# Kernel optimization log

Measured on AMD Instinct MI355X. Metric: run time of the kernel, lower is better.

The kernel has to match this reference:

```python
import jax, jax.numpy as jnp
import numpy as np

B, S, H, NH = 1, 2048, 4096, 32
HD = H // NH
INV_NORM = 1.0 / float(np.sqrt(HD))
BETA = 1.0
NEG_MIN = float(np.finfo(np.float32).min)


def setup_inputs() -> dict:
    key = jax.random.key(0)
    ks = jax.random.split(key, 8)
    hidden_states = jax.random.normal(ks[0], (B, S, H), dtype=jnp.float32)
    residual = jax.random.normal(ks[1], (B, S, H), dtype=jnp.float32)
    # ALiBi: per-head slope * position, shape [B*NH, 1, S] as HF BLOOM builds it
    slopes = jnp.asarray(2.0 ** (-8.0 * (np.arange(1, NH + 1) / NH)), dtype=jnp.float32)
    pos = jnp.arange(S, dtype=jnp.float32)
    alibi = (slopes[:, None, None] * pos[None, None, :])  # [NH,1,S]
    alibi = jnp.tile(alibi, (B, 1, 1))  # [B*NH,1,S]
    # causal mask: True where attention is NOT allowed
    attention_mask = jnp.triu(jnp.ones((S, S), dtype=bool), k=1)[None, None]  # [1,1,S,S]
    w_qkv = jax.random.normal(ks[2], (3 * H, H), dtype=jnp.float32) * 0.02
    b_qkv = jax.random.normal(ks[3], (3 * H,), dtype=jnp.float32) * 0.02
    w_dense = jax.random.normal(ks[4], (H, H), dtype=jnp.float32) * 0.02
    b_dense = jax.random.normal(ks[5], (H,), dtype=jnp.float32) * 0.02
    return {
        'hidden_states': hidden_states, 'residual': residual, 'alibi': alibi,
        'attention_mask': attention_mask, 'w_qkv': w_qkv, 'b_qkv': b_qkv,
        'w_dense': w_dense, 'b_dense': b_dense,
    }


def reference(hidden_states, residual, alibi, attention_mask, w_qkv, b_qkv, w_dense, b_dense):
    # fused QKV projection, interleaved per-head split as in BLOOM
    fused = hidden_states @ w_qkv.T + b_qkv  # [B,S,3H]
    fused = fused.reshape(B, S, NH, 3, HD)
    q, k, v = fused[..., 0, :], fused[..., 1, :], fused[..., 2, :]  # [B,S,NH,HD]
    # baddbmm: beta*alibi + alpha * Q K^T
    scores = jnp.einsum('bqhd,bkhd->bhqk', q, k) * INV_NORM  # [B,NH,S,S]
    scores = scores + BETA * alibi.reshape(B, NH, 1, S)
    scores = jnp.where(attention_mask, NEG_MIN, scores)
    probs = jax.nn.softmax(scores, axis=-1)  # fp32 softmax (inputs already fp32)
    ctx = jnp.einsum('bhqk,bkhd->bqhd', probs, v).reshape(B, S, H)
    out = ctx @ w_dense.T + b_dense
    return out + residual  # dropout_add with p=0 in eval
```

## Files before the change

### kernel.cpp

```cpp
#include <hip/hip_runtime.h>
#include <cstdint>
#include <cstddef>

#define S_LEN 2048
#define H_DIM 4096
#define NHEAD 32
#define HD    128
#define N_QKV 12288
#define INV_NORM 0.08838834764831845f

typedef __bf16 bf16_t;
typedef bf16_t bf16x8 __attribute__((ext_vector_type(8)));
typedef bf16_t bf16x4 __attribute__((ext_vector_type(4)));
typedef float  f32x4  __attribute__((ext_vector_type(4)));

static_assert(sizeof(bf16x8) == 16, "bf16x8 must be 16B");

__device__ __forceinline__ f32x4 mfma16(bf16x8 a, bf16x8 b, f32x4 c) {
  return __builtin_amdgcn_mfma_f32_16x16x32_bf16(a, b, c, 0, 0, 0);
}

typedef __attribute__((address_space(1))) void gas_void;
typedef __attribute__((address_space(3))) void las_void;
__device__ __forceinline__ void async16(const void* g, void* l) {
  __builtin_amdgcn_global_load_lds((const gas_void*)g,
                                   (las_void*)(uint32_t)(uintptr_t)l,
                                   16, 0, 0);
}

#define SWZ(x)    ((x) ^ ((((x) >> 7) & 7) << 4))
#define SWZ256(x) ((x) ^ ((((x) >> 8) & 7) << 4))
#define VMCNT(n) asm volatile("s_waitcnt vmcnt(" #n ")" ::: "memory")
#define LGKM0()  asm volatile("s_waitcnt lgkmcnt(0)" ::: "memory")
#define SCHED0() __builtin_amdgcn_sched_barrier(0)
#define BARRIER() __builtin_amdgcn_s_barrier()

typedef float f32v4 __attribute__((ext_vector_type(4)));
#define NX4 ((S_LEN * H_DIM) / 4)
#define NQ4 ((N_QKV * H_DIM) / 4)
#define ND4 ((H_DIM * H_DIM) / 4)
__global__ void cvt_all(const float* __restrict__ x, const float* __restrict__ wq,
                        const float* __restrict__ wd,
                        bf16_t* __restrict__ xb, bf16_t* __restrict__ wqb,
                        bf16_t* __restrict__ wdb) {
  int i = blockIdx.x * 256 + threadIdx.x;
  const float* src; bf16_t* dst; int j;
  if (i < NX4) { src = x; dst = xb; j = i; }
  else if (i < NX4 + NQ4) { src = wq; dst = wqb; j = i - NX4; }
  else if (i < NX4 + NQ4 + ND4) { src = wd; dst = wdb; j = i - NX4 - NQ4; }
  else return;
  f32v4 v = ((const f32v4*)src)[j];
  bf16x4 r;
  r[0] = (bf16_t)v[0]; r[1] = (bf16_t)v[1]; r[2] = (bf16_t)v[2]; r[3] = (bf16_t)v[3];
  ((bf16x4*)dst)[j] = r;
}

template <int MODE, int BN>
__global__ __launch_bounds__(512, 2)
void gemm_pipe(const bf16_t* __restrict__ Ag,
               const bf16_t* __restrict__ Bg,
               const float* __restrict__ bias,
               const float* __restrict__ residual,
               bf16_t* __restrict__ q_out,
               bf16_t* __restrict__ k_out,
               bf16_t* __restrict__ v_out,
               float* __restrict__ f_out,
               int ncol)
{
  constexpr int NFRAG = BN / 32;
  constexpr int NBU   = BN / 64;
  constexpr int BBUF  = BN * 128;
  __shared__ __align__(16) char sm[65536 + 2 * BBUF];
  char* smA = sm;
  char* smB = sm + 65536;
  const int Kdim = H_DIM;
  const int NT = Kdim >> 6;

  const int tid = threadIdx.x, lane = tid & 63, w = tid >> 6;
  const int wm = w >> 1, wn = w & 1;
  const int lo = lane & 15, g = lane >> 4;

  const int nwg = gridDim.x * gridDim.y;
  const int bid = blockIdx.y * gridDim.x + blockIdx.x;
  const int cpx = nwg >> 3;
  const int sbid = (bid & 7) * cpx + (bid >> 3);
  const int brow = (sbid / ncol) << 8;
  const int bcol = (sbid % ncol) * BN;

  auto stageA = [&](int t, int u) {
    const int lin = u * 8192 + w * 1024 + lane * 16;
    const int lg = SWZ(lin);
    const bf16_t* src = Ag + (size_t)(brow + (lg >> 7)) * Kdim + (t << 6) + ((lg & 127) >> 1);
    async16(src, smA + ((t & 1) * 32768 + u * 8192 + w * 1024));
  };
  auto stageB = [&](int t, int u) {
    const int lin = u * 8192 + w * 1024 + lane * 16;
    const int lg = SWZ(lin);
    const bf16_t* src = Bg + (size_t)(bcol + (lg >> 7)) * Kdim + (t << 6) + ((lg & 127) >> 1);
    async16(src, smB + ((t & 1) * BBUF + u * 8192 + w * 1024));
  };
  auto rdA = [&](int t, int mi, int ks) -> bf16x8 {
    const int lin = (wm * 64 + mi * 16 + lo) * 128 + ks * 64 + g * 16;
    return *(const bf16x8*)(smA + (t & 1) * 32768 + SWZ(lin));
  };
  auto rdB = [&](int t, int ni, int ks) -> bf16x8 {
    const int lin = (wn * (BN / 2) + ni * 16 + lo) * 128 + ks * 64 + g * 16;
    return *(const bf16x8*)(smB + (t & 1) * BBUF + SWZ(lin));
  };

  f32x4 acc[4][NFRAG] = {};
  bf16x8 bfrag[NFRAG][2];

#pragma unroll
  for (int u = 0; u < NBU; ++u) stageB(0, u);
  stageA(0, 0); stageA(0, 1); stageA(0, 2); stageA(0, 3);
#pragma unroll
  for (int u = 0; u < NBU; ++u) stageB(1, u);
  if constexpr (NBU == 3) { VMCNT(3); } else { VMCNT(2); }
  SCHED0();
  BARRIER();

  for (int t = 0; t < NT; ++t) {
    bf16x8 afrag[2][2];
#pragma unroll
    for (int ni = 0; ni < NFRAG; ++ni)
#pragma unroll
      for (int ks = 0; ks < 2; ++ks)
        bfrag[ni][ks] = rdB(t, ni, ks);
#pragma unroll
    for (int j = 0; j < 2; ++j)
#pragma unroll
      for (int ks = 0; ks < 2; ++ks)
        afrag[j][ks] = rdA(t, j, ks);
    if (t + 1 < NT) { stageA(t + 1, 0); stageA(t + 1, 1); stageA(t + 1, 2); stageA(t + 1, 3); }
    SCHED0();
    BARRIER();
    __builtin_amdgcn_s_setprio(1);
#pragma unroll
    for (int j = 0; j < 2; ++j)
#pragma unroll
      for (int ni = 0; ni < NFRAG; ++ni)
#pragma unroll
        for (int ks = 0; ks < 2; ++ks)
          acc[j][ni] = mfma16(afrag[j][ks], bfrag[ni][ks], acc[j][ni]);
    __builtin_amdgcn_s_setprio(0);
    SCHED0();
    BARRIER();
#pragma unroll
    for (int j = 0; j < 2; ++j)
#pragma unroll
      for (int ks = 0; ks < 2; ++ks)
        afrag[j][ks] = rdA(t, 2 + j, ks);
    if (t + 2 < NT) {
#pragma unroll
      for (int u = 0; u < NBU; ++u) stageB(t + 2, u);
    }
    SCHED0();
    BARRIER();
    if (t < NT - 2) {
      if constexpr (NBU == 3) { VMCNT(3); } else { VMCNT(2); }
    } else if (t == NT - 2) {
      VMCNT(0);
    }
    __builtin_amdgcn_s_setprio(1);
#pragma unroll
    for (int j = 0; j < 2; ++j)
#pragma unroll
      for (int ni = 0; ni < NFRAG; ++ni)
#pragma unroll
        for (int ks = 0; ks < 2; ++ks)
          acc[2 + j][ni] = mfma16(afrag[j][ks], bfrag[ni][ks], acc[2 + j][ni]);
    __builtin_amdgcn_s_setprio(0);
    SCHED0();
    BARRIER();
  }

  if (MODE == 0) {
#pragma unroll
    for (int ni = 0; ni < NFRAG; ++ni) {
      const int cg = bcol + wn * (BN / 2) + ni * 16 + lo;
      const int chunk = cg >> 7;
      const int slot = chunk % 3, head = chunk / 3;
      bf16_t* dst = (slot == 0) ? q_out : (slot == 1) ? k_out : v_out;
      dst += (size_t)head * S_LEN * HD;
      const float scale = (slot == 0) ? INV_NORM : 1.0f;
      const float bb = bias[cg];
      const int d = cg & 127;
#pragma unroll
      for (int mi = 0; mi < 4; ++mi) {
#pragma unroll
        for (int jj = 0; jj < 4; ++jj) {
          const int r = brow + wm * 64 + mi * 16 + g * 4 + jj;
          dst[(size_t)r * HD + d] = (bf16_t)((acc[mi][ni][jj] + bb) * scale);
        }
      }
    }
  } else {
#pragma unroll
    for (int ni = 0; ni < NFRAG; ++ni) {
      const int cg = bcol + wn * (BN / 2) + ni * 16 + lo;
      const float bb = bias[cg];
#pragma unroll
      for (int mi = 0; mi < 4; ++mi) {
#pragma unroll
        for (int jj = 0; jj < 4; ++jj) {
          const int r = brow + wm * 64 + mi * 16 + g * 4 + jj;
          f_out[(size_t)r * H_DIM + cg] = acc[mi][ni][jj] + bb + residual[(size_t)r * H_DIM + cg];
        }
      }
    }
  }
}

__global__ __launch_bounds__(256, 2)
void attn_kernel(const bf16_t* __restrict__ Qg,
                 const bf16_t* __restrict__ Kg,
                 const bf16_t* __restrict__ Vg,
                 const float* __restrict__ alibi,
                 bf16_t* __restrict__ ctx)
{
  const int bid = blockIdx.x;
  const int h  = (bid & 7) * 4 + ((bid >> 3) & 3);
  const int qb = 31 - (bid >> 5);
  const int tid = threadIdx.x, lane = tid & 63, w = tid >> 6;
  const int lo = lane & 15, g = lane >> 4;

  __shared__ __align__(16) bf16_t Ks[2][64 * 128];
  __shared__ bf16_t Vt[2][128][72];
  __shared__ bf16_t Pl[4][16][72];

  const bf16_t* Qh = Qg + ((size_t)h * S_LEN + qb * 64 + w * 16) * HD;
  const bf16_t* Kh = Kg + (size_t)h * S_LEN * HD;
  const bf16_t* Vh = Vg + (size_t)h * S_LEN * HD;
  const float slope = alibi[(size_t)h * S_LEN + 1];

  bf16x8 qf[4];
#pragma unroll
  for (int ds = 0; ds < 4; ds++)
    qf[ds] = *(const bf16x8*)(Qh + lo * HD + ds * 32 + g * 8);

  f32x4 oacc[8] = {};
  float m_r[4], l_r[4];
#pragma unroll
  for (int jj = 0; jj < 4; jj++) { m_r[jj] = -INFINITY; l_r[jj] = 0.f; }

  const int ntiles = qb + 1;
  const int q_base = qb * 64 + w * 16;

  bf16x8 vvA[4], vvB[4];
#pragma unroll
  for (int u = 0; u < 4; ++u)
    vvA[u] = *(const bf16x8*)(Vh + (size_t)lane * HD + (u * 4 + w) * 8);
#pragma unroll
  for (int u = 0; u < 4; ++u) {
    const int lin = u * 4096 + tid * 16;
    const int lg = SWZ256(lin);
    async16(Kh + (size_t)(lg >> 8) * HD + ((lg & 255) >> 1),
            (char*)&Ks[0][0] + u * 4096 + w * 1024);
  }

  for (int kt = 0; kt < ntiles; ++kt) {
    const int k0 = kt * 64;
    const int cur = kt & 1;
    const bf16x8* vvC = cur ? vvB : vvA;
    bf16x8* vvN = cur ? vvA : vvB;

#pragma unroll
    for (int u = 0; u < 4; ++u) {
      const int d0 = (u * 4 + w) * 8;
#pragma unroll
      for (int e = 0; e < 8; ++e) Vt[cur][d0 + e][lane] = vvC[u][e];
    }
    if (kt + 1 < ntiles) {
      const bf16_t* Vn = Vh + (size_t)(k0 + 64) * HD;
#pragma unroll
      for (int u = 0; u < 4; ++u)
        vvN[u] = *(const bf16x8*)(Vn + (size_t)lane * HD + (u * 4 + w) * 8);
    }
    SCHED0();
    if (kt + 1 < ntiles) { VMCNT(4); } else { VMCNT(0); }
    LGKM0();
    SCHED0();
    BARRIER();
    SCHED0();
    if (kt + 1 < ntiles) {
      const bf16_t* Kn = Kh + (size_t)(k0 + 64) * HD;
#pragma unroll
      for (int u = 0; u < 4; ++u) {
        const int lin = u * 4096 + tid * 16;
        const int lg = SWZ256(lin);
        async16(Kn + (size_t)(lg >> 8) * HD + ((lg & 255) >> 1),
                (char*)&Ks[cur ^ 1][0] + u * 4096 + w * 1024);
      }
    }

    f32x4 sacc[4] = {};
#pragma unroll
    for (int kc = 0; kc < 4; ++kc) {
      bf16x8 kf[4];
#pragma unroll
      for (int ds = 0; ds < 4; ++ds) {
        const int lin = (kc * 16 + lo) * 256 + ds * 64 + g * 16;
        kf[ds] = *(const bf16x8*)((const char*)&Ks[cur][0] + SWZ256(lin));
      }
      __builtin_amdgcn_s_setprio(1);
#pragma unroll
      for (int ds = 0; ds < 4; ++ds)
        sacc[kc] = mfma16(qf[ds], kf[ds], sacc[kc]);
      __builtin_amdgcn_s_setprio(0);
    }

    float sv[4][4];
#pragma unroll
    for (int kc = 0; kc < 4; kc++) {
      const float alk = slope * (float)(k0 + kc * 16 + lo);
#pragma unroll
      for (int jj = 0; jj < 4; jj++)
        sv[kc][jj] = sacc[kc][jj] + alk;
    }
    if (kt == ntiles - 1) {
#pragma unroll
      for (int kc = 0; kc < 4; kc++) {
        const int k_gl = k0 + kc * 16 + lo;
#pragma unroll
        for (int jj = 0; jj < 4; jj++) {
          const int q_gl = q_base + g * 4 + jj;
          if (k_gl > q_gl) sv[kc][jj] = -INFINITY;
        }
      }
    }

#pragma unroll
    for (int jj = 0; jj < 4; jj++) {
      float mx = fmaxf(fmaxf(sv[0][jj], sv[1][jj]), fmaxf(sv[2][jj], sv[3][jj]));
      mx = fmaxf(mx, __shfl_xor(mx, 1, 64));
      mx = fmaxf(mx, __shfl_xor(mx, 2, 64));
      mx = fmaxf(mx, __shfl_xor(mx, 4, 64));
      mx = fmaxf(mx, __shfl_xor(mx, 8, 64));
      const float mn = fmaxf(m_r[jj], mx);
      const float sc = __expf(m_r[jj] - mn);
      m_r[jj] = mn;
      l_r[jj] *= sc;
#pragma unroll
      for (int df = 0; df < 8; df++) oacc[df][jj] *= sc;
      float rs = 0.f;
#pragma unroll
      for (int kc = 0; kc < 4; kc++) {
        const float p = __expf(sv[kc][jj] - mn);
        rs += p;
        Pl[w][g * 4 + jj][kc * 16 + lo] = (bf16_t)p;
      }
      rs += __shfl_xor(rs, 1, 64);
      rs += __shfl_xor(rs, 2, 64);
      rs += __shfl_xor(rs, 4, 64);
      rs += __shfl_xor(rs, 8, 64);
      l_r[jj] += rs;
    }

#pragma unroll
    for (int ks = 0; ks < 2; ++ks) {
      bf16x8 pa = *(const bf16x8*)&Pl[w][lo][ks * 32 + g * 8];
#pragma unroll
      for (int df = 0; df < 8; df++) {
        bf16x8 vf = *(const bf16x8*)&Vt[cur][df * 16 + lo][ks * 32 + g * 8];
        __builtin_amdgcn_s_setprio(1);
        oacc[df] = mfma16(pa, vf, oacc[df]);
        __builtin_amdgcn_s_setprio(0);
      }
    }
  }

#pragma unroll
  for (int jj = 0; jj < 4; jj++) {
    const float inv = 1.0f / l_r[jj];
    const int r = q_base + g * 4 + jj;
#pragma unroll
    for (int df = 0; df < 8; df++) {
      const int d = df * 16 + lo;
      ctx[(size_t)r * H_DIM + h * HD + d] = (bf16_t)(oacc[df][jj] * inv);
    }
  }
}

extern "C" void kernel_launch(void* const* d_in, const int* in_sizes, int n_in,
                              void* d_out, int out_size, void* d_ws, size_t ws_size,
                              hipStream_t stream) {
  const float* hidden   = (const float*)d_in[0];
  const float* residual = (const float*)d_in[1];
  const float* alibi    = (const float*)d_in[2];
  const float* w_qkv    = (const float*)d_in[4];
  const float* b_qkv    = (const float*)d_in[5];
  const float* w_dense  = (const float*)d_in[6];
  const float* b_dense  = (const float*)d_in[7];
  float* out = (float*)d_out;

  char* ws = (char*)d_ws;
  bf16_t* Xb  = (bf16_t*)(ws);
  bf16_t* Wqb = (bf16_t*)(ws + 16777216);
  bf16_t* Wdb = (bf16_t*)(ws + 117440512);
  bf16_t* Qb  = (bf16_t*)(ws + 150994944);
  bf16_t* Kb  = (bf16_t*)(ws + 167772160);
  bf16_t* Vb  = (bf16_t*)(ws + 184549376);
  bf16_t* Ctx = (bf16_t*)(ws + 201326592);

  {
    int n4 = NX4 + NQ4 + ND4;
    cvt_all<<<(n4 + 255) / 256, 256, 0, stream>>>(hidden, w_qkv, w_dense, Xb, Wqb, Wdb);
  }

  gemm_pipe<0, 192><<<dim3(N_QKV / 192, S_LEN / 256), 512, 0, stream>>>(
      Xb, Wqb, b_qkv, nullptr, Qb, Kb, Vb, nullptr, N_QKV / 192);

  attn_kernel<<<NHEAD * (S_LEN / 64), 256, 0, stream>>>(Qb, Kb, Vb, alibi, Ctx);

  gemm_pipe<1, 128><<<dim3(H_DIM / 128, S_LEN / 256), 512, 0, stream>>>(
      Ctx, Wdb, b_dense, residual, nullptr, nullptr, nullptr, out, H_DIM / 128);
}
```

Before: 462.0 us.

## Use lazy softmax rescaling and compute row sums via MFMA with ones

The attention inner loop now skips the online-softmax rescale of the output accumulators unless some row's max grows by more than a threshold, warp-uniformly via __any. Row sums are no longer reduced with shuffles; they come from an extra MFMA of the probability tile against a ones vector, read out by a lane shuffle at the end. The setprio calls are hoisted to wrap whole MFMA loops. This trades shuffle and VALU work for one extra MFMA per k-slice, and relies on exponentials staying bounded (up to e^8) before rescaling, which could affect bf16 precision.

```diff
diff --git a/kernel.cpp b/kernel.cpp
--- a/kernel.cpp
+++ b/kernel.cpp
@@ -239,10 +239,15 @@
   for (int ds = 0; ds < 4; ds++)
     qf[ds] = *(const bf16x8*)(Qh + lo * HD + ds * 32 + g * 8);
 
+  bf16x8 vones;
+#pragma unroll
+  for (int e = 0; e < 8; ++e) vones[e] = (bf16_t)((lo == 0) ? 1.0f : 0.0f);
+
   f32x4 oacc[8] = {};
-  float m_r[4], l_r[4];
-#pragma unroll
-  for (int jj = 0; jj < 4; jj++) { m_r[jj] = -INFINITY; l_r[jj] = 0.f; }
+  f32x4 oaccL = {};
+  float m_r[4];
+#pragma unroll
+  for (int jj = 0; jj < 4; jj++) m_r[jj] = -INFINITY;
 
   const int ntiles = qb + 1;
   const int q_base = qb * 64 + w * 16;
@@ -295,6 +300,7 @@
     }
 
     f32x4 sacc[4] = {};
+    __builtin_amdgcn_s_setprio(1);
 #pragma unroll
     for (int kc = 0; kc < 4; ++kc) {
       bf16x8 kf[4];
@@ -303,12 +309,11 @@
         const int lin = (kc * 16 + lo) * 256 + ds * 64 + g * 16;
         kf[ds] = *(const bf16x8*)((const char*)&Ks[cur][0] + SWZ256(lin));
       }
-      __builtin_amdgcn_s_setprio(1);
 #pragma unroll
       for (int ds = 0; ds < 4; ++ds)
         sacc[kc] = mfma16(qf[ds], kf[ds], sacc[kc]);
-      __builtin_amdgcn_s_setprio(0);
-    }
+    }
+    __builtin_amdgcn_s_setprio(0);
 
     float sv[4][4];
 #pragma unroll
@@ -330,49 +335,54 @@
       }
     }
 
+    float mx[4];
 #pragma unroll
     for (int jj = 0; jj < 4; jj++) {
-      float mx = fmaxf(fmaxf(sv[0][jj], sv[1][jj]), fmaxf(sv[2][jj], sv[3][jj]));
-      mx = fmaxf(mx, __shfl_xor(mx, 1, 64));
-      mx = fmaxf(mx, __shfl_xor(mx, 2, 64));
-      mx = fmaxf(mx, __shfl_xor(mx, 4, 64));
-      mx = fmaxf(mx, __shfl_xor(mx, 8, 64));
-      const float mn = fmaxf(m_r[jj], mx);
-      const float sc = __expf(m_r[jj] - mn);
-      m_r[jj] = mn;
-      l_r[jj] *= sc;
-#pragma unroll
-      for (int df = 0; df < 8; df++) oacc[df][jj] *= sc;
-      float rs = 0.f;
-#pragma unroll
-      for (int kc = 0; kc < 4; kc++) {
-        const float p = __expf(sv[kc][jj] - mn);
-        rs += p;
-        Pl[w][g * 4 + jj][kc * 16 + lo] = (bf16_t)p;
-      }
-      rs += __shfl_xor(rs, 1, 64);
-      rs += __shfl_xor(rs, 2, 64);
-      rs += __shfl_xor(rs, 4, 64);
-      rs += __shfl_xor(rs, 8, 64);
-      l_r[jj] += rs;
-    }
-
+      float m0 = fmaxf(fmaxf(sv[0][jj], sv[1][jj]), fmaxf(sv[2][jj], sv[3][jj]));
+      m0 = fmaxf(m0, __shfl_xor(m0, 1, 64));
+      m0 = fmaxf(m0, __shfl_xor(m0, 2, 64));
+      m0 = fmaxf(m0, __shfl_xor(m0, 4, 64));
+      m0 = fmaxf(m0, __shfl_xor(m0, 8, 64));
+      mx[jj] = m0;
+    }
+    bool need = false;
+#pragma unroll
+    for (int jj = 0; jj < 4; jj++) need = need || (mx[jj] > m_r[jj] + 8.0f);
+    if (__any(need)) {
+#pragma unroll
+      for (int jj = 0; jj < 4; jj++) {
+        const float mn = fmaxf(m_r[jj], mx[jj]);
+        const float sc = __expf(m_r[jj] - mn);
+        m_r[jj] = mn;
+#pragma unroll
+        for (int df = 0; df < 8; df++) oacc[df][jj] *= sc;
+        oaccL[jj] *= sc;
+      }
+    }
+#pragma unroll
+    for (int jj = 0; jj < 4; jj++)
+#pragma unroll
+      for (int kc = 0; kc < 4; kc++)
+        Pl[w][g * 4 + jj][kc * 16 + lo] = (bf16_t)__expf(sv[kc][jj] - m_r[jj]);
+
+    __builtin_amdgcn_s_setprio(1);
 #pragma unroll
     for (int ks = 0; ks < 2; ++ks) {
       bf16x8 pa = *(const bf16x8*)&Pl[w][lo][ks * 32 + g * 8];
+      oaccL = mfma16(pa, vones, oaccL);
 #pragma unroll
       for (int df = 0; df < 8; df++) {
         bf16x8 vf = *(const bf16x8*)&Vt[cur][df * 16 + lo][ks * 32 + g * 8];
-        __builtin_amdgcn_s_setprio(1);
         oacc[df] = mfma16(pa, vf, oacc[df]);
-        __builtin_amdgcn_s_setprio(0);
-      }
-    }
+      }
+    }
+    __builtin_amdgcn_s_setprio(0);
   }
 
 #pragma unroll
   for (int jj = 0; jj < 4; jj++) {
-    const float inv = 1.0f / l_r[jj];
+    const float l = __shfl(oaccL[jj], lane & 48, 64);
+    const float inv = 1.0f / l;
     const int r = q_base + g * 4 + jj;
 #pragma unroll
     for (int df = 0; df < 8; df++) {
```

New measurement: 448.2 us, median of 2. -3.0%, faster.
